# Kernel optimization log

Measured on AMD Instinct MI355X. Metric: run time of the kernel, lower is better.

Reference implementation:

```python
import jax, jax.numpy as jnp
import numpy as np

D_MODEL = 768
HEADS = 12
HEAD_DIM = D_MODEL // HEADS


def setup_inputs() -> dict:
    key = jax.random.key(0)
    ks = jax.random.split(key, 5)
    B, L = 4, 2048
    x = jax.random.normal(ks[0], (B, L, D_MODEL), dtype=jnp.float32)
    # torch nn.Linear init scale ~ 1/sqrt(fan_in); use small random weights
    s = 1.0 / np.sqrt(D_MODEL)
    W_qkv = jax.random.uniform(ks[1], (D_MODEL, 3 * D_MODEL), jnp.float32, -s, s)
    b_qkv = jax.random.uniform(ks[2], (3 * D_MODEL,), jnp.float32, -s, s)
    W_out = jax.random.uniform(ks[3], (D_MODEL, D_MODEL), jnp.float32, -s, s)
    b_out = jax.random.uniform(ks[4], (D_MODEL,), jnp.float32, -s, s)
    return {"x": x, "W_qkv": W_qkv, "b_qkv": b_qkv, "W_out": W_out, "b_out": b_out}


def reference(x, W_qkv, b_qkv, W_out, b_out):
    B, L, D = x.shape
    scale = jnp.sqrt(jnp.float32(HEAD_DIM))
    # qkv projection: [B, L, 3*D] -> [3, B, heads, L, head_dim]
    qkv = (x @ W_qkv + b_qkv).reshape(B, L, 3, HEADS, HEAD_DIM)
    qkv = jnp.transpose(qkv, (2, 0, 3, 1, 4))
    q, k, v = qkv[0], qkv[1], qkv[2]
    # full materialized attention, no mask
    scores = jnp.einsum("bhld,bhmd->bhlm", q, k) / scale  # [B, H, L, L]
    attn = jax.nn.softmax(scores, axis=-1)
    out = jnp.einsum("bhlm,bhmd->bhld", attn, v)  # [B, H, L, head_dim]
    out = jnp.transpose(out, (0, 2, 1, 3)).reshape(B, L, D)
    return out @ W_out + b_out
```

## Files before the change

### kernel.cpp

```cpp
#include <hip/hip_runtime.h>
#include <cmath>

typedef __bf16 bf16_t;
typedef __bf16 bf16x8 __attribute__((ext_vector_type(8)));
typedef __bf16 bf16x4 __attribute__((ext_vector_type(4)));
typedef short s16x4 __attribute__((ext_vector_type(4)));
typedef float f32x4 __attribute__((ext_vector_type(4)));

#define MFMA(a, b, c) __builtin_amdgcn_mfma_f32_16x16x32_bf16((a), (b), (c), 0, 0, 0)
#if __has_builtin(__builtin_amdgcn_mfma_f32_16x16x16_bf16)
#define MFMA16(a, b, c) __builtin_amdgcn_mfma_f32_16x16x16_bf16((a), (b), (c), 0, 0, 0)
#else
#define MFMA16(a, b, c)                                                              \
  __builtin_amdgcn_mfma_f32_16x16x16bf16_1k(__builtin_bit_cast(s16x4, (bf16x4)(a)), \
                                            __builtin_bit_cast(s16x4, (bf16x4)(b)), (c), 0, 0, 0)
#endif

static constexpr int D = 768;
static constexpr int L = 2048;
static constexpr int NB = 4;
static constexpr int NH = 12;
static constexpr int HD = 64;
static constexpr int M = 8192;
static constexpr int NQKV = 2304;
#define QSCALE 0.18033688011112042f

__device__ __forceinline__ void glds16(const bf16_t* g, bf16_t* l) {
  __builtin_amdgcn_global_load_lds((const __attribute__((address_space(1))) void*)g,
                                   (__attribute__((address_space(3))) void*)l, 16, 0, 0);
}

__global__ __launch_bounds__(256) void cvt_bf16_kernel(const float* __restrict__ in,
                                                       bf16_t* __restrict__ out, int n8) {
  int g = blockIdx.x * 256 + threadIdx.x;
  if (g >= n8) return;
  const float4* p = (const float4*)in + (size_t)g * 2;
  float4 a = p[0], b = p[1];
  bf16x8 v = {(__bf16)a.x, (__bf16)a.y, (__bf16)a.z, (__bf16)a.w,
              (__bf16)b.x, (__bf16)b.y, (__bf16)b.z, (__bf16)b.w};
  *(bf16x8*)(out + (size_t)g * 8) = v;
}

__global__ __launch_bounds__(256) void transpose_cvt_kernel(const float* __restrict__ in,
                                                            bf16_t* __restrict__ out,
                                                            int rows, int cols) {
  __shared__ float t[32][33];
  int c0 = blockIdx.x * 32, r0 = blockIdx.y * 32;
  int tx = threadIdx.x, ty = threadIdx.y;
  for (int i = ty; i < 32; i += 8) t[i][tx] = in[(size_t)(r0 + i) * cols + c0 + tx];
  __syncthreads();
  for (int i = ty; i < 32; i += 8) out[(size_t)(c0 + i) * rows + r0 + tx] = (__bf16)t[tx][i];
}

__global__ __launch_bounds__(256) void gemm_qkv_kernel(const bf16_t* __restrict__ A,
                                                       const bf16_t* __restrict__ Bt,
                                                       const float* __restrict__ bias,
                                                       bf16_t* __restrict__ Qo,
                                                       bf16_t* __restrict__ Ko,
                                                       bf16_t* __restrict__ Vto) {
  __shared__ __align__(16) bf16_t As[128 * 32];
  __shared__ __align__(16) bf16_t Bs[128 * 32];
  const int tid = threadIdx.x;
  const int wave = tid >> 6, lane = tid & 63;
  const int quad = lane >> 4, l16 = lane & 15;
  const int wm = (wave >> 1) * 64, wn = (wave & 1) * 64;
  const int tm = blockIdx.x * 128, tn = blockIdx.y * 128;
  const int lr = tid >> 2, lc = (tid & 3) * 8;
  const bf16_t* Ag = A + (size_t)(tm + lr) * D + lc;
  const bf16_t* Bg = Bt + (size_t)(tn + lr) * D + lc;
  bf16_t* lA0 = &As[wave * 512];
  bf16_t* lA1 = &As[2048 + wave * 512];
  bf16_t* lB0 = &Bs[wave * 512];
  bf16_t* lB1 = &Bs[2048 + wave * 512];
  f32x4 acc[4][4] = {};
  for (int kt = 0; kt < D; kt += 32) {
    __syncthreads();
    glds16(Ag + kt, lA0);
    glds16(Ag + (size_t)64 * D + kt, lA1);
    glds16(Bg + kt, lB0);
    glds16(Bg + (size_t)64 * D + kt, lB1);
    __syncthreads();
    bf16x8 af[4], bfr[4];
#pragma unroll
    for (int i = 0; i < 4; i++) af[i] = *(const bf16x8*)&As[(wm + i * 16 + l16) * 32 + quad * 8];
#pragma unroll
    for (int j = 0; j < 4; j++) bfr[j] = *(const bf16x8*)&Bs[(wn + j * 16 + l16) * 32 + quad * 8];
#pragma unroll
    for (int i = 0; i < 4; i++)
#pragma unroll
      for (int j = 0; j < 4; j++) acc[i][j] = MFMA(af[i], bfr[j], acc[i][j]);
  }
#pragma unroll
  for (int i = 0; i < 4; i++)
#pragma unroll
    for (int j = 0; j < 4; j++) {
      int n = tn + wn + j * 16 + l16;
      float bn = bias[n];
      int which = n / 768, rem = n - which * 768;
      int h = rem >> 6, d = rem & 63;
      int m0 = tm + wm + i * 16 + quad * 4;
      int b0 = m0 >> 11, l0 = m0 & 2047;
      int bh = b0 * NH + h;
      if (which == 2) {
        bf16x4 w;
#pragma unroll
        for (int r2 = 0; r2 < 4; r2++) w[r2] = (__bf16)(acc[i][j][r2] + bn);
        *(bf16x4*)&Vto[((size_t)bh * HD + d) * L + l0] = w;
      } else if (which == 0) {
#pragma unroll
        for (int r2 = 0; r2 < 4; r2++)
          Qo[((size_t)bh * L + l0 + r2) * HD + d] = (__bf16)((acc[i][j][r2] + bn) * QSCALE);
      } else {
#pragma unroll
        for (int r2 = 0; r2 < 4; r2++)
          Ko[((size_t)bh * L + l0 + r2) * HD + d] = (__bf16)(acc[i][j][r2] + bn);
      }
    }
}

__global__ __launch_bounds__(256) void attn_kernel(const bf16_t* __restrict__ Q,
                                                   const bf16_t* __restrict__ K,
                                                   const bf16_t* __restrict__ Vt,
                                                   bf16_t* __restrict__ O) {
  __shared__ __align__(16) bf16_t Ks[64][72];
  __shared__ __align__(16) bf16_t Vs[64][72];
  const int tid = threadIdx.x;
  const int wave = tid >> 6, lane = tid & 63;
  const int quad = lane >> 4, l16 = lane & 15;
  const int bh = blockIdx.y;
  const int q0 = blockIdx.x * 128 + wave * 32;
  const bf16_t* Kb = K + (size_t)bh * L * HD;
  const bf16_t* Vb = Vt + (size_t)bh * HD * L;
  bf16x8 bq[2][2];
#pragma unroll
  for (int g = 0; g < 2; g++) {
    const bf16_t* Qp = Q + ((size_t)bh * L + q0 + g * 16 + l16) * HD + quad * 8;
    bq[g][0] = *(const bf16x8*)Qp;
    bq[g][1] = *(const bf16x8*)(Qp + 32);
  }
  f32x4 oacc[2][4] = {};
  float lacc[2] = {0.f, 0.f};
  const int st = tid >> 3, sc = (tid & 7) * 8;
  for (int j = 0; j < L / 64; j++) {
    int kv0 = j * 64;
    __syncthreads();
    *(bf16x8*)&Ks[st][sc] = *(const bf16x8*)(Kb + (size_t)(kv0 + st) * HD + sc);
    *(bf16x8*)&Ks[st + 32][sc] = *(const bf16x8*)(Kb + (size_t)(kv0 + st + 32) * HD + sc);
    *(bf16x8*)&Vs[st][sc] = *(const bf16x8*)(Vb + (size_t)st * L + kv0 + sc);
    *(bf16x8*)&Vs[st + 32][sc] = *(const bf16x8*)(Vb + (size_t)(st + 32) * L + kv0 + sc);
    __syncthreads();
    f32x4 s[2][4];
#pragma unroll
    for (int fn = 0; fn < 4; fn++) {
      bf16x8 ak0 = *(const bf16x8*)&Ks[fn * 16 + l16][quad * 8];
      bf16x8 ak1 = *(const bf16x8*)&Ks[fn * 16 + l16][32 + quad * 8];
#pragma unroll
      for (int g = 0; g < 2; g++) {
        f32x4 z = {};
        z = MFMA(ak0, bq[g][0], z);
        s[g][fn] = MFMA(ak1, bq[g][1], z);
      }
    }
    bf16x4 pb[2][4];
#pragma unroll
    for (int g = 0; g < 2; g++)
#pragma unroll
      for (int fn = 0; fn < 4; fn++) {
        float e0 = exp2f(s[g][fn][0]), e1 = exp2f(s[g][fn][1]);
        float e2 = exp2f(s[g][fn][2]), e3 = exp2f(s[g][fn][3]);
        lacc[g] += (e0 + e1) + (e2 + e3);
        bf16x4 w = {(__bf16)e0, (__bf16)e1, (__bf16)e2, (__bf16)e3};
        pb[g][fn] = w;
      }
#pragma unroll
    for (int fd = 0; fd < 4; fd++)
#pragma unroll
      for (int fn = 0; fn < 4; fn++) {
        bf16x4 av = *(const bf16x4*)&Vs[fd * 16 + l16][fn * 16 + quad * 4];
#pragma unroll
        for (int g = 0; g < 2; g++) oacc[g][fd] = MFMA16(av, pb[g][fn], oacc[g][fd]);
      }
  }
  const int b = bh / NH, h = bh - b * NH;
#pragma unroll
  for (int g = 0; g < 2; g++) {
    float ls = lacc[g];
    ls += __shfl_xor(ls, 16, 64);
    ls += __shfl_xor(ls, 32, 64);
    float rinv = 1.f / ls;
    int row = q0 + g * 16 + l16;
    bf16_t* Op = O + ((size_t)(b * L + row)) * D + h * HD;
#pragma unroll
    for (int fd = 0; fd < 4; fd++) {
      bf16x4 w;
#pragma unroll
      for (int r = 0; r < 4; r++) w[r] = (__bf16)(oacc[g][fd][r] * rinv);
      *(bf16x4*)(Op + fd * 16 + quad * 4) = w;
    }
  }
}

__global__ __launch_bounds__(256) void gemm_out_kernel(const bf16_t* __restrict__ A,
                                                       const bf16_t* __restrict__ Bt,
                                                       const float* __restrict__ bias,
                                                       float* __restrict__ Cg) {
  __shared__ __align__(16) bf16_t As[128 * 32];
  __shared__ __align__(16) bf16_t Bs[128 * 32];
  const int tid = threadIdx.x;
  const int wave = tid >> 6, lane = tid & 63;
  const int quad = lane >> 4, l16 = lane & 15;
  const int wm = (wave >> 1) * 64, wn = (wave & 1) * 64;
  const int tm = blockIdx.x * 128, tn = blockIdx.y * 128;
  const int lr = tid >> 2, lc = (tid & 3) * 8;
  const bf16_t* Ag = A + (size_t)(tm + lr) * D + lc;
  const bf16_t* Bg = Bt + (size_t)(tn + lr) * D + lc;
  bf16_t* lA0 = &As[wave * 512];
  bf16_t* lA1 = &As[2048 + wave * 512];
  bf16_t* lB0 = &Bs[wave * 512];
  bf16_t* lB1 = &Bs[2048 + wave * 512];
  f32x4 acc[4][4] = {};
  for (int kt = 0; kt < D; kt += 32) {
    __syncthreads();
    glds16(Ag + kt, lA0);
    glds16(Ag + (size_t)64 * D + kt, lA1);
    glds16(Bg + kt, lB0);
    glds16(Bg + (size_t)64 * D + kt, lB1);
    __syncthreads();
    bf16x8 af[4], bfr[4];
#pragma unroll
    for (int i = 0; i < 4; i++) af[i] = *(const bf16x8*)&As[(wm + i * 16 + l16) * 32 + quad * 8];
#pragma unroll
    for (int j = 0; j < 4; j++) bfr[j] = *(const bf16x8*)&Bs[(wn + j * 16 + l16) * 32 + quad * 8];
#pragma unroll
    for (int i = 0; i < 4; i++)
#pragma unroll
      for (int j = 0; j < 4; j++) acc[i][j] = MFMA(af[i], bfr[j], acc[i][j]);
  }
#pragma unroll
  for (int i = 0; i < 4; i++)
#pragma unroll
    for (int j = 0; j < 4; j++) {
      int n = tn + wn + j * 16 + l16;
      float bn = bias[n];
#pragma unroll
      for (int r2 = 0; r2 < 4; r2++) {
        int m = tm + wm + i * 16 + quad * 4 + r2;
        Cg[(size_t)m * D + n] = acc[i][j][r2] + bn;
      }
    }
}

extern "C" void kernel_launch(void* const* d_in, const int* in_sizes, int n_in,
                              void* d_out, int out_size, void* d_ws, size_t ws_size,
                              hipStream_t stream) {
  const float* x = (const float*)d_in[0];
  const float* Wqkv = (const float*)d_in[1];
  const float* bqkv = (const float*)d_in[2];
  const float* Wout = (const float*)d_in[3];
  const float* bout = (const float*)d_in[4];
  float* out = (float*)d_out;

  bf16_t* xb = (bf16_t*)d_ws;
  bf16_t* wqT = xb + (size_t)M * D;
  bf16_t* woT = wqT + (size_t)NQKV * D;
  bf16_t* Qb = woT + (size_t)D * D;
  bf16_t* Kb = Qb + (size_t)M * D;
  bf16_t* Vtb = Kb + (size_t)M * D;
  bf16_t* Ob = Vtb + (size_t)M * D;

  cvt_bf16_kernel<<<(M * D / 8 + 255) / 256, 256, 0, stream>>>(x, xb, M * D / 8);
  transpose_cvt_kernel<<<dim3(NQKV / 32, D / 32), dim3(32, 8), 0, stream>>>(Wqkv, wqT, D, NQKV);
  transpose_cvt_kernel<<<dim3(D / 32, D / 32), dim3(32, 8), 0, stream>>>(Wout, woT, D, D);
  gemm_qkv_kernel<<<dim3(M / 128, NQKV / 128), 256, 0, stream>>>(xb, wqT, bqkv, Qb, Kb, Vtb);
  attn_kernel<<<dim3(L / 128, NB * NH), 256, 0, stream>>>(Qb, Kb, Vtb, Ob);
  gemm_out_kernel<<<dim3(M / 128, D / 128), 256, 0, stream>>>(Ob, woT, bout, out);
}
```

Before: 261.7 us.

## Prefetch next K/V tile into registers and permute V layout for wide LDS reads

```diff
diff --git a/kernel.cpp b/kernel.cpp
--- a/kernel.cpp
+++ b/kernel.cpp
@@ -102,10 +102,12 @@
       int b0 = m0 >> 11, l0 = m0 & 2047;
       int bh = b0 * NH + h;
       if (which == 2) {
+        int l6 = l0 & 63;
+        int lp = (l0 & ~63) | (((l6 >> 2) & 3) * 16) | ((l6 >> 4) * 4);
         bf16x4 w;
 #pragma unroll
         for (int r2 = 0; r2 < 4; r2++) w[r2] = (__bf16)(acc[i][j][r2] + bn);
-        *(bf16x4*)&Vto[((size_t)bh * HD + d) * L + l0] = w;
+        *(bf16x4*)&Vto[((size_t)bh * HD + d) * L + lp] = w;
       } else if (which == 0) {
 #pragma unroll
         for (int r2 = 0; r2 < 4; r2++)
@@ -141,14 +143,24 @@
   f32x4 oacc[2][4] = {};
   float lacc[2] = {0.f, 0.f};
   const int st = tid >> 3, sc = (tid & 7) * 8;
+  bf16x8 pk0 = *(const bf16x8*)(Kb + (size_t)st * HD + sc);
+  bf16x8 pk1 = *(const bf16x8*)(Kb + (size_t)(st + 32) * HD + sc);
+  bf16x8 pv0 = *(const bf16x8*)(Vb + (size_t)st * L + sc);
+  bf16x8 pv1 = *(const bf16x8*)(Vb + (size_t)(st + 32) * L + sc);
   for (int j = 0; j < L / 64; j++) {
-    int kv0 = j * 64;
-    __syncthreads();
-    *(bf16x8*)&Ks[st][sc] = *(const bf16x8*)(Kb + (size_t)(kv0 + st) * HD + sc);
-    *(bf16x8*)&Ks[st + 32][sc] = *(const bf16x8*)(Kb + (size_t)(kv0 + st + 32) * HD + sc);
-    *(bf16x8*)&Vs[st][sc] = *(const bf16x8*)(Vb + (size_t)st * L + kv0 + sc);
-    *(bf16x8*)&Vs[st + 32][sc] = *(const bf16x8*)(Vb + (size_t)(st + 32) * L + kv0 + sc);
-    __syncthreads();
+    __syncthreads();
+    *(bf16x8*)&Ks[st][sc] = pk0;
+    *(bf16x8*)&Ks[st + 32][sc] = pk1;
+    *(bf16x8*)&Vs[st][sc] = pv0;
+    *(bf16x8*)&Vs[st + 32][sc] = pv1;
+    __syncthreads();
+    if (j + 1 < L / 64) {
+      int kv0n = (j + 1) * 64;
+      pk0 = *(const bf16x8*)(Kb + (size_t)(kv0n + st) * HD + sc);
+      pk1 = *(const bf16x8*)(Kb + (size_t)(kv0n + st + 32) * HD + sc);
+      pv0 = *(const bf16x8*)(Vb + (size_t)st * L + kv0n + sc);
+      pv1 = *(const bf16x8*)(Vb + (size_t)(st + 32) * L + kv0n + sc);
+    }
     f32x4 s[2][4];
 #pragma unroll
     for (int fn = 0; fn < 4; fn++) {
@@ -175,10 +187,15 @@
 #pragma unroll
     for (int fd = 0; fd < 4; fd++)
 #pragma unroll
-      for (int fn = 0; fn < 4; fn++) {
-        bf16x4 av = *(const bf16x4*)&Vs[fd * 16 + l16][fn * 16 + quad * 4];
-#pragma unroll
-        for (int g = 0; g < 2; g++) oacc[g][fd] = MFMA16(av, pb[g][fn], oacc[g][fd]);
+      for (int t = 0; t < 2; t++) {
+        bf16x8 av2 = *(const bf16x8*)&Vs[fd * 16 + l16][quad * 16 + t * 8];
+        bf16x4 av0 = {av2[0], av2[1], av2[2], av2[3]};
+        bf16x4 av1 = {av2[4], av2[5], av2[6], av2[7]};
+#pragma unroll
+        for (int g = 0; g < 2; g++) {
+          oacc[g][fd] = MFMA16(av0, pb[g][2 * t], oacc[g][fd]);
+          oacc[g][fd] = MFMA16(av1, pb[g][2 * t + 1], oacc[g][fd]);
+        }
       }
   }
   const int b = bh / NH, h = bh - b * NH;
```

Measured after the change: 244.9 us. -6.4%, faster.
